# Kernel optimization log

Hardware: AMD Instinct MI355X
Metric: run time of the kernel (lower is better)

The kernel has to match this reference:

```python
import jax, jax.numpy as jnp
import numpy as np

SIGMA = 0.25  # self.sigmas in RBFDynamics


def setup_inputs() -> dict:
    key = jax.random.key(0)
    k1, k2, k3 = jax.random.split(key, 3)
    N, C, D, M = 100000, 256, 2, 5
    x = jax.random.normal(k1, (N, D), dtype=jnp.float32)
    centers = jax.random.normal(k2, (C, D), dtype=jnp.float32)
    weights = jax.random.normal(k3, (M, C, D), dtype=jnp.float32)
    return {"x": x, "centers": centers, "weights": weights}


def reference(x, centers, weights):
    x2 = jnp.sum(x * x, axis=-1, keepdims=True)          # [N, 1]
    c2 = jnp.sum(centers * centers, axis=-1)             # [C]
    d2 = x2 + c2[None, :] - 2.0 * (x @ centers.T)        # [N, C]
    d2 = jnp.maximum(d2, 0.0)
    # torch: exp(-cdist(x, centers)**2) * sigmas**2
    rbf = jnp.exp(-d2) * (SIGMA * SIGMA)                 # [N, C]
    # per-model matmul with weights, batched across ensemble -> [M, N, D]
    out = jnp.einsum('nc,mcd->mnd', rbf, weights)
    return out
```

## Files before the change

### kernel.cpp

```cpp
#include <hip/hip_runtime.h>

#if __has_builtin(__builtin_amdgcn_exp2f)
__device__ __forceinline__ float fast_exp2(float x) { return __builtin_amdgcn_exp2f(x); }
#else
__device__ __forceinline__ float fast_exp2(float x) { return exp2f(x); }
#endif

constexpr int C_ = 256;
constexpr int D_ = 2;
constexpr int M_ = 5;
constexpr float LOG2E = 1.4426950408889634f;

__global__ __launch_bounds__(256) void ensemble_rbf_kernel(
    const float* __restrict__ x,
    const float* __restrict__ centers,
    const float* __restrict__ weights,
    float* __restrict__ out,
    int N)
{
    __shared__ float2 s_ctr[C_];
    __shared__ float4 s_w[C_][3];

    const int tid = threadIdx.x;

    s_ctr[tid] = ((const float2*)centers)[tid];

    float* wf = (float*)s_w;
    for (int i = tid; i < M_ * C_ * D_; i += 256) {
        int m = i >> 9;
        int r = i & 511;
        int c = r >> 1;
        int d = r & 1;
        wf[c * 12 + m * 2 + d] = weights[i];
    }
    __syncthreads();

    const int n = blockIdx.x * 256 + tid;
    if (n >= N) return;

    const float2 xv = ((const float2*)x)[n];

    float accx[M_], accy[M_];
    #pragma unroll
    for (int m = 0; m < M_; m++) { accx[m] = 0.f; accy[m] = 0.f; }

    #pragma unroll 4
    for (int c = 0; c < C_; c++) {
        float2 ctr = s_ctr[c];
        float dx = xv.x - ctr.x;
        float dy = xv.y - ctr.y;
        float d2 = fmaf(dx, dx, dy * dy);
        float r = fast_exp2(fmaf(d2, -LOG2E, -4.0f));

        float4 w0 = s_w[c][0];
        float4 w1 = s_w[c][1];
        float4 w2 = s_w[c][2];
        accx[0] = fmaf(r, w0.x, accx[0]);  accy[0] = fmaf(r, w0.y, accy[0]);
        accx[1] = fmaf(r, w0.z, accx[1]);  accy[1] = fmaf(r, w0.w, accy[1]);
        accx[2] = fmaf(r, w1.x, accx[2]);  accy[2] = fmaf(r, w1.y, accy[2]);
        accx[3] = fmaf(r, w1.z, accx[3]);  accy[3] = fmaf(r, w1.w, accy[3]);
        accx[4] = fmaf(r, w2.x, accx[4]);  accy[4] = fmaf(r, w2.y, accy[4]);
    }

    float2* out2 = (float2*)out;
    #pragma unroll
    for (int m = 0; m < M_; m++) {
        out2[(size_t)m * N + n] = make_float2(accx[m], accy[m]);
    }
}

extern "C" void kernel_launch(void* const* d_in, const int* in_sizes, int n_in,
                              void* d_out, int out_size, void* d_ws, size_t ws_size,
                              hipStream_t stream) {
    const float* x       = (const float*)d_in[0];
    const float* centers = (const float*)d_in[1];
    const float* weights = (const float*)d_in[2];
    float* out = (float*)d_out;

    int N = in_sizes[0] / 2;
    int grid = (N + 255) / 256;
    ensemble_rbf_kernel<<<grid, 256, 0, stream>>>(x, centers, weights, out, N);
}
```

Measured before the change: 75.61 us.

## Split center loop across four wavefronts and reduce partial sums in LDS

Each block now handles 64 points, and its four wavefronts each process a quarter of the 256 centers. Partial accumulators are combined through shared memory before one wavefront writes the output. Centers and weights are packed into a single interleaved LDS table, and the block fills it with coalesced loads. This creates four times as many blocks, which is meant to improve occupancy and load balance across CUs. The cost is an extra reduction phase, two more barriers, and the table setup being repeated by four times as many blocks.

```diff
diff --git a/kernel.cpp b/kernel.cpp
--- a/kernel.cpp
+++ b/kernel.cpp
@@ -7,7 +7,6 @@
 #endif
 
 constexpr int C_ = 256;
-constexpr int D_ = 2;
 constexpr int M_ = 5;
 constexpr float LOG2E = 1.4426950408889634f;
 
@@ -18,54 +17,82 @@
     float* __restrict__ out,
     int N)
 {
-    __shared__ float2 s_ctr[C_];
-    __shared__ float4 s_w[C_][3];
+    __shared__ float s_tab[C_ * 12];
 
-    const int tid = threadIdx.x;
+    const int tid   = threadIdx.x;
+    const int nl    = tid & 63;
+    const int chunk = tid >> 6;
 
-    s_ctr[tid] = ((const float2*)centers)[tid];
-
-    float* wf = (float*)s_w;
-    for (int i = tid; i < M_ * C_ * D_; i += 256) {
-        int m = i >> 9;
-        int r = i & 511;
-        int c = r >> 1;
-        int d = r & 1;
-        wf[c * 12 + m * 2 + d] = weights[i];
+    {
+        float2 cv = ((const float2*)centers)[tid];
+        float* row = &s_tab[tid * 12];
+        row[0] = cv.x;
+        row[1] = cv.y;
+        const float2* w2 = (const float2*)weights;
+        #pragma unroll
+        for (int m = 0; m < M_; m++) {
+            float2 wv = w2[m * C_ + tid];
+            row[2 + 2 * m]     = wv.x;
+            row[2 + 2 * m + 1] = wv.y;
+        }
     }
     __syncthreads();
 
-    const int n = blockIdx.x * 256 + tid;
-    if (n >= N) return;
-
-    const float2 xv = ((const float2*)x)[n];
+    const int n = blockIdx.x * 64 + nl;
+    float2 xv = (n < N) ? ((const float2*)x)[n] : make_float2(0.f, 0.f);
 
     float accx[M_], accy[M_];
     #pragma unroll
     for (int m = 0; m < M_; m++) { accx[m] = 0.f; accy[m] = 0.f; }
 
-    #pragma unroll 4
-    for (int c = 0; c < C_; c++) {
-        float2 ctr = s_ctr[c];
-        float dx = xv.x - ctr.x;
-        float dy = xv.y - ctr.y;
+    const float4* tab4 = (const float4*)s_tab;
+    const int cbase = chunk * 64;
+
+    #pragma unroll 8
+    for (int cc = 0; cc < 64; cc++) {
+        int c = cbase + cc;
+        float4 t0 = tab4[c * 3 + 0];
+        float4 t1 = tab4[c * 3 + 1];
+        float4 t2 = tab4[c * 3 + 2];
+
+        float dx = xv.x - t0.x;
+        float dy = xv.y - t0.y;
         float d2 = fmaf(dx, dx, dy * dy);
-        float r = fast_exp2(fmaf(d2, -LOG2E, -4.0f));
+        float r  = fast_exp2(fmaf(d2, -LOG2E, -4.0f));
 
-        float4 w0 = s_w[c][0];
-        float4 w1 = s_w[c][1];
-        float4 w2 = s_w[c][2];
-        accx[0] = fmaf(r, w0.x, accx[0]);  accy[0] = fmaf(r, w0.y, accy[0]);
-        accx[1] = fmaf(r, w0.z, accx[1]);  accy[1] = fmaf(r, w0.w, accy[1]);
-        accx[2] = fmaf(r, w1.x, accx[2]);  accy[2] = fmaf(r, w1.y, accy[2]);
-        accx[3] = fmaf(r, w1.z, accx[3]);  accy[3] = fmaf(r, w1.w, accy[3]);
-        accx[4] = fmaf(r, w2.x, accx[4]);  accy[4] = fmaf(r, w2.y, accy[4]);
+        accx[0] = fmaf(r, t0.z, accx[0]);  accy[0] = fmaf(r, t0.w, accy[0]);
+        accx[1] = fmaf(r, t1.x, accx[1]);  accy[1] = fmaf(r, t1.y, accy[1]);
+        accx[2] = fmaf(r, t1.z, accx[2]);  accy[2] = fmaf(r, t1.w, accy[2]);
+        accx[3] = fmaf(r, t2.x, accx[3]);  accy[3] = fmaf(r, t2.y, accy[3]);
+        accx[4] = fmaf(r, t2.z, accx[4]);  accy[4] = fmaf(r, t2.w, accy[4]);
     }
 
-    float2* out2 = (float2*)out;
-    #pragma unroll
-    for (int m = 0; m < M_; m++) {
-        out2[(size_t)m * N + n] = make_float2(accx[m], accy[m]);
+    __syncthreads();
+    {
+        float4* slot = (float4*)&s_tab[(chunk * 64 + nl) * 12];
+        slot[0] = make_float4(accx[0], accy[0], accx[1], accy[1]);
+        slot[1] = make_float4(accx[2], accy[2], accx[3], accy[3]);
+        slot[2] = make_float4(accx[4], accy[4], 0.f, 0.f);
+    }
+    __syncthreads();
+
+    if (tid < 64 && n < N) {
+        float4 s0 = make_float4(0.f, 0.f, 0.f, 0.f);
+        float4 s1 = s0, s2 = s0;
+        #pragma unroll
+        for (int k = 0; k < 4; k++) {
+            const float4* slot = (const float4*)&s_tab[(k * 64 + nl) * 12];
+            float4 r0 = slot[0], r1 = slot[1], r2 = slot[2];
+            s0.x += r0.x; s0.y += r0.y; s0.z += r0.z; s0.w += r0.w;
+            s1.x += r1.x; s1.y += r1.y; s1.z += r1.z; s1.w += r1.w;
+            s2.x += r2.x; s2.y += r2.y;
+        }
+        float2* out2 = (float2*)out;
+        out2[(size_t)0 * N + n] = make_float2(s0.x, s0.y);
+        out2[(size_t)1 * N + n] = make_float2(s0.z, s0.w);
+        out2[(size_t)2 * N + n] = make_float2(s1.x, s1.y);
+        out2[(size_t)3 * N + n] = make_float2(s1.z, s1.w);
+        out2[(size_t)4 * N + n] = make_float2(s2.x, s2.y);
     }
 }
 
@@ -78,6 +105,6 @@
     float* out = (float*)d_out;
 
     int N = in_sizes[0] / 2;
-    int grid = (N + 255) / 256;
+    int grid = (N + 63) / 64;
     ensemble_rbf_kernel<<<grid, 256, 0, stream>>>(x, centers, weights, out, N);
 }
```

Measured after the change: 70.63 us (median of 2 runs). 1.07x faster.

## Use packed fp16 dot2 for RBF-weight accumulation with center-split reduction

Applied to the files above, without the earlier changes.

Converts the RBF values and the ensemble weights to packed fp16 pairs, so that each v_dot2 instruction accumulates two centers into an fp32 accumulator. Each block now handles 128 points with 4 groups of 64 threads, each group covering 64 centers, and the partial sums are reduced through shared memory before the output store. This is meant to cut the FMA count per point roughly in half and amortize the shared-memory loads over two points per thread. The cost is fp16 rounding of the RBF values and weights, an extra shared-memory reduction with two more barriers, and the plain exp2f call replacing the amdgcn builtin.

```diff
diff --git a/kernel.cpp b/kernel.cpp
--- a/kernel.cpp
+++ b/kernel.cpp
@@ -1,15 +1,25 @@
 #include <hip/hip_runtime.h>
 
-#if __has_builtin(__builtin_amdgcn_exp2f)
-__device__ __forceinline__ float fast_exp2(float x) { return __builtin_amdgcn_exp2f(x); }
-#else
-__device__ __forceinline__ float fast_exp2(float x) { return exp2f(x); }
-#endif
+typedef _Float16 half2_t __attribute__((ext_vector_type(2)));
+typedef __fp16   fp16v2  __attribute__((ext_vector_type(2)));
 
 constexpr int C_ = 256;
-constexpr int D_ = 2;
-constexpr int M_ = 5;
 constexpr float LOG2E = 1.4426950408889634f;
+
+union F4H8 { float4 f4; half2_t h2[4]; float2 f2[2]; };
+union H2U  { fp16v2 p; half2_t h; };
+
+__device__ __forceinline__ half2_t pack2(float a, float b) {
+    H2U u; u.p = __builtin_amdgcn_cvt_pkrtz(a, b); return u.h;
+}
+
+__device__ __forceinline__ float dot2acc(half2_t a, half2_t b, float c) {
+#if __has_builtin(__builtin_amdgcn_fdot2)
+    return __builtin_amdgcn_fdot2(a, b, c, false);
+#else
+    return c + (float)a.x * (float)b.x + (float)a.y * (float)b.y;
+#endif
+}
 
 __global__ __launch_bounds__(256) void ensemble_rbf_kernel(
     const float* __restrict__ x,
@@ -18,54 +28,123 @@
     float* __restrict__ out,
     int N)
 {
-    __shared__ float2 s_ctr[C_];
-    __shared__ float4 s_w[C_][3];
+    __shared__ float4 smem4[1536];
 
-    const int tid = threadIdx.x;
+    const int tid   = threadIdx.x;
+    const int nl    = tid & 63;
+    const int chunk = tid >> 6;
 
-    s_ctr[tid] = ((const float2*)centers)[tid];
-
-    float* wf = (float*)s_w;
-    for (int i = tid; i < M_ * C_ * D_; i += 256) {
-        int m = i >> 9;
-        int r = i & 511;
-        int c = r >> 1;
-        int d = r & 1;
-        wf[c * 12 + m * 2 + d] = weights[i];
+    if (tid < 128) {
+        const int p = tid;
+        float4 ctr = ((const float4*)centers)[p];
+        const float4* w4 = (const float4*)weights;
+        F4H8 uA, uB, uC;
+        #pragma unroll
+        for (int m = 0; m < 5; m++) {
+            float4 q = w4[m * 128 + p];
+            half2_t h0 = pack2(q.x, q.z);
+            half2_t h1 = pack2(q.y, q.w);
+            int j0 = 2 * m, j1 = 2 * m + 1;
+            if (j0 < 4) uA.h2[j0] = h0; else if (j0 < 8) uB.h2[j0 - 4] = h0; else uC.h2[j0 - 8] = h0;
+            if (j1 < 4) uA.h2[j1] = h1; else if (j1 < 8) uB.h2[j1 - 4] = h1; else uC.h2[j1 - 8] = h1;
+        }
+        uC.h2[2] = pack2(0.f, 0.f);
+        uC.h2[3] = uC.h2[2];
+        smem4[p * 4 + 0] = ctr;
+        smem4[p * 4 + 1] = uA.f4;
+        smem4[p * 4 + 2] = uB.f4;
+        smem4[p * 4 + 3] = uC.f4;
     }
     __syncthreads();
 
-    const int n = blockIdx.x * 256 + tid;
-    if (n >= N) return;
+    const int base = blockIdx.x * 128;
+    const int n0 = base + nl;
+    const int n1 = n0 + 64;
+    const float2* x2 = (const float2*)x;
+    float2 xv0 = x2[min(n0, N - 1)];
+    float2 xv1 = x2[min(n1, N - 1)];
 
-    const float2 xv = ((const float2*)x)[n];
+    float a0[10], a1[10];
+    #pragma unroll
+    for (int j = 0; j < 10; j++) { a0[j] = 0.f; a1[j] = 0.f; }
 
-    float accx[M_], accy[M_];
-    #pragma unroll
-    for (int m = 0; m < M_; m++) { accx[m] = 0.f; accy[m] = 0.f; }
+    const int pbase = chunk * 32;
 
     #pragma unroll 4
-    for (int c = 0; c < C_; c++) {
-        float2 ctr = s_ctr[c];
-        float dx = xv.x - ctr.x;
-        float dy = xv.y - ctr.y;
-        float d2 = fmaf(dx, dx, dy * dy);
-        float r = fast_exp2(fmaf(d2, -LOG2E, -4.0f));
+    for (int pp = 0; pp < 32; pp++) {
+        int p = pbase + pp;
+        float4 ctr = smem4[p * 4 + 0];
+        F4H8 uA, uB;
+        uA.f4 = smem4[p * 4 + 1];
+        uB.f4 = smem4[p * 4 + 2];
+        float2 wc = *((const float2*)&smem4[p * 4 + 3]);
+        F4H8 uC; uC.f2[0] = wc;
 
-        float4 w0 = s_w[c][0];
-        float4 w1 = s_w[c][1];
-        float4 w2 = s_w[c][2];
-        accx[0] = fmaf(r, w0.x, accx[0]);  accy[0] = fmaf(r, w0.y, accy[0]);
-        accx[1] = fmaf(r, w0.z, accx[1]);  accy[1] = fmaf(r, w0.w, accy[1]);
-        accx[2] = fmaf(r, w1.x, accx[2]);  accy[2] = fmaf(r, w1.y, accy[2]);
-        accx[3] = fmaf(r, w1.z, accx[3]);  accy[3] = fmaf(r, w1.w, accy[3]);
-        accx[4] = fmaf(r, w2.x, accx[4]);  accy[4] = fmaf(r, w2.y, accy[4]);
+        float dx, dy, d2;
+        dx = xv0.x - ctr.x; dy = xv0.y - ctr.y; d2 = fmaf(dx, dx, dy * dy);
+        float r00 = exp2f(fmaf(d2, -LOG2E, -4.0f));
+        dx = xv0.x - ctr.z; dy = xv0.y - ctr.w; d2 = fmaf(dx, dx, dy * dy);
+        float r01 = exp2f(fmaf(d2, -LOG2E, -4.0f));
+        dx = xv1.x - ctr.x; dy = xv1.y - ctr.y; d2 = fmaf(dx, dx, dy * dy);
+        float r10 = exp2f(fmaf(d2, -LOG2E, -4.0f));
+        dx = xv1.x - ctr.z; dy = xv1.y - ctr.w; d2 = fmaf(dx, dx, dy * dy);
+        float r11 = exp2f(fmaf(d2, -LOG2E, -4.0f));
+
+        half2_t rp0 = pack2(r00, r01);
+        half2_t rp1 = pack2(r10, r11);
+
+        #pragma unroll
+        for (int j = 0; j < 4; j++) {
+            a0[j] = dot2acc(rp0, uA.h2[j], a0[j]);
+            a1[j] = dot2acc(rp1, uA.h2[j], a1[j]);
+        }
+        #pragma unroll
+        for (int j = 0; j < 4; j++) {
+            a0[4 + j] = dot2acc(rp0, uB.h2[j], a0[4 + j]);
+            a1[4 + j] = dot2acc(rp1, uB.h2[j], a1[4 + j]);
+        }
+        a0[8] = dot2acc(rp0, uC.h2[0], a0[8]);
+        a1[8] = dot2acc(rp1, uC.h2[0], a1[8]);
+        a0[9] = dot2acc(rp0, uC.h2[1], a0[9]);
+        a1[9] = dot2acc(rp1, uC.h2[1], a1[9]);
     }
 
-    float2* out2 = (float2*)out;
-    #pragma unroll
-    for (int m = 0; m < M_; m++) {
-        out2[(size_t)m * N + n] = make_float2(accx[m], accy[m]);
+    __syncthreads();
+    float* smemf = (float*)smem4;
+    {
+        float* row0 = &smemf[(chunk * 128 + nl) * 12];
+        ((float4*)row0)[0] = make_float4(a0[0], a0[1], a0[2], a0[3]);
+        ((float4*)row0)[1] = make_float4(a0[4], a0[5], a0[6], a0[7]);
+        ((float2*)row0)[4] = make_float2(a0[8], a0[9]);
+        float* row1 = &smemf[(chunk * 128 + 64 + nl) * 12];
+        ((float4*)row1)[0] = make_float4(a1[0], a1[1], a1[2], a1[3]);
+        ((float4*)row1)[1] = make_float4(a1[4], a1[5], a1[6], a1[7]);
+        ((float2*)row1)[4] = make_float2(a1[8], a1[9]);
+    }
+    __syncthreads();
+
+    if (tid < 128) {
+        const int n = base + tid;
+        if (n < N) {
+            float s[10];
+            #pragma unroll
+            for (int j = 0; j < 10; j++) s[j] = 0.f;
+            #pragma unroll
+            for (int k = 0; k < 4; k++) {
+                const float* row = &smemf[(k * 128 + tid) * 12];
+                float4 r0 = ((const float4*)row)[0];
+                float4 r1 = ((const float4*)row)[1];
+                float2 r2 = ((const float2*)row)[4];
+                s[0] += r0.x; s[1] += r0.y; s[2] += r0.z; s[3] += r0.w;
+                s[4] += r1.x; s[5] += r1.y; s[6] += r1.z; s[7] += r1.w;
+                s[8] += r2.x; s[9] += r2.y;
+            }
+            float2* out2 = (float2*)out;
+            #pragma unroll
+            for (int m = 0; m < 5; m++) {
+                out2[(size_t)m * N + n] = make_float2(s[2 * m], s[2 * m + 1]);
+            }
+        }
     }
 }
 
@@ -78,6 +157,6 @@
     float* out = (float*)d_out;
 
     int N = in_sizes[0] / 2;
-    int grid = (N + 255) / 256;
+    int grid = (N + 127) / 128;
     ensemble_rbf_kernel<<<grid, 256, 0, stream>>>(x, centers, weights, out, N);
 }
```

New measurement: 74.96 us. Within noise of the previous version (-0.9%).
